# Performance work log

Measured on AMD Instinct MI355X. Metric: run time of the kernel, lower is better.

## Reference

```python
import jax, jax.numpy as jnp
import numpy as np

EPS = 1e-5
K = 16
D = 2

def _bn(x, gamma, beta):
    # eval-mode BatchNorm with running_mean=0, running_var=1
    return x * (gamma / jnp.sqrt(1.0 + EPS)) + beta

def _dense(x, W, b, gamma=None, beta=None, act=True):
    y = x @ W + b
    if act:
        y = jax.nn.elu(y)
    if gamma is not None:
        y = _bn(y, gamma, beta)
    return y

def setup_inputs() -> dict:
    key = jax.random.key(0)
    ks = jax.random.split(key, 16)
    N, Npts, P, dims = 16, 8192, 2048, 3
    C_in, C_out = 64, 128
    C_mid = C_out // 4      # 32
    C_half = C_out // 2     # 64
    dm = 2                  # depth_multiplier = min(ceil(C_out/C_in), 4)
    Ccat = C_mid + C_half   # 96
    def w(k, shape, fan_in):
        return (jax.random.normal(k, shape, jnp.float32) / np.float32(np.sqrt(fan_in)))
    return {
        "rep_pts": jax.random.normal(ks[0], (N, P, dims), jnp.float32),
        "pts": jax.random.normal(ks[1], (N, Npts, dims), jnp.float32),
        "fts": jax.random.normal(ks[2], (N, Npts, C_in), jnp.float32),
        "pts_idx": jax.random.randint(ks[3], (N, P, K * D), 0, Npts),
        # PointCNN.dense: C_in -> C_out//2 (Linear+ELU+BN)
        "dense_W": w(ks[4], (C_in, C_half), C_in), "dense_b": jnp.zeros(C_half),
        "dense_g": jnp.ones(C_half), "dense_bt": jnp.zeros(C_half),
        # XConv dense1/dense2: dims->C_mid->C_mid
        "d1_W": w(ks[5], (dims, C_mid), dims), "d1_b": jnp.zeros(C_mid),
        "d1_g": jnp.ones(C_mid), "d1_bt": jnp.zeros(C_mid),
        "d2_W": w(ks[6], (C_mid, C_mid), C_mid), "d2_b": jnp.zeros(C_mid),
        "d2_g": jnp.ones(C_mid), "d2_bt": jnp.zeros(C_mid),
        "xt_cW": w(ks[7], (K * K, dims, K), dims * K), "xt_cb": jnp.zeros(K * K),
        "xt_d1W": w(ks[8], (K * K, K * K), K * K), "xt_d1b": jnp.zeros(K * K),
        "xt_d2W": w(ks[9], (K * K, K * K), K * K), "xt_d2b": jnp.zeros(K * K),
        # end_conv SepConv: depthwise (1,K) with depth_multiplier, then pointwise 1x1
        "dw_W": w(ks[10], (Ccat, dm, K), K), "dw_b": jnp.zeros(Ccat * dm),
        "pw_W": w(ks[11], (Ccat * dm, C_out), Ccat * dm), "pw_b": jnp.zeros(C_out),
        "sep_g": jnp.ones(C_out), "sep_bt": jnp.zeros(C_out),
    }

def reference(rep_pts, pts, fts, pts_idx,
              dense_W, dense_b, dense_g, dense_bt,
              d1_W, d1_b, d1_g, d1_bt,
              d2_W, d2_b, d2_g, d2_bt,
              xt_cW, xt_cb, xt_d1W, xt_d1b, xt_d2W, xt_d2b,
              dw_W, dw_b, pw_W, pw_b, sep_g, sep_bt):
    idx = pts_idx[:, :, : K * D : D]                  # [N,P,K]
    gather = jax.vmap(lambda a, i: a[i])              # per-batch neighbor gather
    # fts -> Dense(C_in, C_out//2)
    fts_l = _dense(fts, dense_W, dense_b, dense_g, dense_bt)
    pts_reg = gather(pts, idx)                        # [N,P,K,dims]
    fts_reg = gather(fts_l, idx)                      # [N,P,K,C_half]
    pts_local = pts_reg - rep_pts[:, :, None, :]      # center neighborhoods
    # lift coordinates to C_mid features
    l0 = _dense(pts_local, d1_W, d1_b, d1_g, d1_bt)
    lifted = _dense(l0, d2_W, d2_b, d2_g, d2_bt)      # [N,P,K,C_mid]
    fts_cat = jnp.concatenate([lifted, fts_reg], axis=-1)  # [N,P,K,Ccat]
    # X-transform: Conv (1,K) over dims -> K*K (ELU, no BN), two Dense (last no act)
    Xc = jax.nn.elu(jnp.einsum('npkd,odk->npo', pts_local, xt_cW) + xt_cb)
    X = jax.nn.elu(Xc @ xt_d1W + xt_d1b)
    X = X @ xt_d2W + xt_d2b
    N_, P_ = X.shape[0], X.shape[1]
    X = X.reshape(N_, P_, K, K)
    fts_X = jnp.einsum('npij,npjc->npic', X, fts_cat)  # [N,P,K,Ccat]
    # depthwise separable conv over K, then ELU + BN, squeeze -> [N,P,C_out]
    dw = jnp.einsum('npkc,cmk->npcm', fts_X, dw_W).reshape(N_, P_, -1) + dw_b
    out = jax.nn.elu(dw @ pw_W + pw_b)
    out = _bn(out, sep_g, sep_bt)
    return out
```

## Files before the change

### kernel.cpp

```cpp
#include <hip/hip_runtime.h>
#include <hip/hip_bf16.h>

#define RS 0.9999950000374998f

__device__ __forceinline__ float eluf(float x) {
    return x > 0.0f ? x : __expf(x) - 1.0f;
}

typedef __attribute__((ext_vector_type(8))) __bf16 bf16x8;
typedef __attribute__((ext_vector_type(4))) float f32x4;
typedef __attribute__((ext_vector_type(4))) unsigned int u32x4;

__global__ __launch_bounds__(256) void gather_kernel(
    const float* __restrict__ rep_pts, const float* __restrict__ pts,
    const int* __restrict__ pts_idx, const float* __restrict__ d1W,
    const float* __restrict__ d2W, const float* __restrict__ pwW,
    const float* __restrict__ d2Ws, const float* __restrict__ denseW,
    const float* __restrict__ cW, float* __restrict__ pts_local,
    __hip_bfloat16* __restrict__ PLB, __hip_bfloat16* __restrict__ d1Wt,
    __hip_bfloat16* __restrict__ d2Wt, __hip_bfloat16* __restrict__ pwWt,
    __hip_bfloat16* __restrict__ d2pWt, __hip_bfloat16* __restrict__ denseWt,
    __hip_bfloat16* __restrict__ cWt) {
    const int tid = threadIdx.x;
    if (blockIdx.x < 256) {
        const int t = blockIdx.x * 256 + tid;
        {
            const int k = t >> 8, n = t & 255;
            d1Wt[n * 256 + k] = __float2bfloat16(d1W[t]);
            d2Wt[n * 256 + k] = __float2bfloat16(d2W[t]);
        }
        if (t < 24576) {
            const int k = t >> 7, n = t & 127;
            pwWt[n * 192 + k] = __float2bfloat16(pwW[t]);
        }
        if (t < 1024) {
            const int q = t >> 5, c = t & 31;
            d2pWt[c * 32 + q] = __float2bfloat16(d2Ws[t]);
        }
        if (t < 4096) {
            const int k = t >> 6, n = t & 63;
            denseWt[n * 64 + k] = __float2bfloat16(denseW[t]);
        }
        if (t < 16384) {
            const int o = t >> 6, kq = t & 63;
            cWt[t] = (kq < 48) ? __float2bfloat16(cW[o * 48 + kq])
                               : __float2bfloat16(0.0f);
        }
    }
    const long gp0 = (long)blockIdx.x * 16;
    const int pt = tid >> 4, k = tid & 15;
    const long gp = gp0 + pt;
    const int n = (int)(gp >> 11);
    const int idx = pts_idx[gp * 32 + 2 * k];
    const float* ps = pts + ((long)n * 8192 + idx) * 3;
    const float* rs = rep_pts + gp * 3;
#pragma unroll
    for (int d = 0; d < 3; ++d) {
        const float v = ps[d] - rs[d];
        pts_local[gp * 48 + k * 3 + d] = v;
        PLB[gp * 64 + d * 16 + k] = __float2bfloat16(v);
    }
    PLB[gp * 64 + 48 + k] = __float2bfloat16(0.0f);
}

__global__ __launch_bounds__(256) void mfma_gemm_f32a64(
    const float* __restrict__ A, const __hip_bfloat16* __restrict__ Wt,
    const float* __restrict__ bias, const float* __restrict__ gamma,
    const float* __restrict__ beta, __hip_bfloat16* __restrict__ outp, int K,
    int Ncols) {
    __shared__ __bf16 As[128][40];
    __shared__ __bf16 Bs[64][40];
    const int tid = threadIdx.x;
    const int w = tid >> 6, l = tid & 63;
    const long row0 = (long)blockIdx.x * 128;
    const int sr = tid >> 1, sh = tid & 1;
    const int fr = l & 15, kg = (l >> 4) * 8;
    f32x4 acc[2][4] = {};
    const float* __restrict__ ap = A + (row0 + sr) * (long)K + sh * 16;
    const __hip_bfloat16* __restrict__ bp = Wt + (long)(sr & 63) * K + sh * 16;
    for (int k0 = 0; k0 < K; k0 += 32) {
        float av[16];
#pragma unroll
        for (int q = 0; q < 4; ++q) {
            const float4 v = *reinterpret_cast<const float4*>(ap + k0 + q * 4);
            av[q * 4 + 0] = v.x;
            av[q * 4 + 1] = v.y;
            av[q * 4 + 2] = v.z;
            av[q * 4 + 3] = v.w;
        }
        union {
            __bf16 b[16];
            uint4 u[2];
        } cv;
#pragma unroll
        for (int e = 0; e < 16; ++e) cv.b[e] = (__bf16)av[e];
        *reinterpret_cast<uint4*>(&As[sr][sh * 16]) = cv.u[0];
        *reinterpret_cast<uint4*>(&As[sr][sh * 16 + 8]) = cv.u[1];
        if (tid < 128) {
            const uint4 bv0 = *reinterpret_cast<const uint4*>(bp + k0);
            const uint4 bv1 = *reinterpret_cast<const uint4*>(bp + k0 + 8);
            *reinterpret_cast<uint4*>(&Bs[sr & 63][sh * 16]) = bv0;
            *reinterpret_cast<uint4*>(&Bs[sr & 63][sh * 16 + 8]) = bv1;
        }
        __syncthreads();
        bf16x8 af[2], bfv[4];
#pragma unroll
        for (int mt = 0; mt < 2; ++mt)
            af[mt] =
                *reinterpret_cast<const bf16x8*>(&As[w * 32 + mt * 16 + fr][kg]);
#pragma unroll
        for (int nt = 0; nt < 4; ++nt)
            bfv[nt] = *reinterpret_cast<const bf16x8*>(&Bs[nt * 16 + fr][kg]);
#pragma unroll
        for (int mt = 0; mt < 2; ++mt)
#pragma unroll
            for (int nt = 0; nt < 4; ++nt)
                acc[mt][nt] = __builtin_amdgcn_mfma_f32_16x16x32_bf16(
                    af[mt], bfv[nt], acc[mt][nt], 0, 0, 0);
        __syncthreads();
    }
    const int rg = (l >> 4) * 4;
#pragma unroll
    for (int nt = 0; nt < 4; ++nt) {
        const int col = nt * 16 + fr;
        const float bb = bias[col];
        const float gs = gamma[col] * RS;
        const float bt = beta[col];
#pragma unroll
        for (int mt = 0; mt < 2; ++mt) {
#pragma unroll
            for (int r = 0; r < 4; ++r) {
                const long row = row0 + w * 32 + mt * 16 + rg + r;
                float v = acc[mt][nt][r] + bb;
                v = eluf(v) * gs + bt;
                outp[row * Ncols + col] = __float2bfloat16(v);
            }
        }
    }
}

__global__ __launch_bounds__(1024) void xchain_kernel(
    const __hip_bfloat16* __restrict__ PLB, const __hip_bfloat16* __restrict__ cWt,
    const float* __restrict__ cb, const __hip_bfloat16* __restrict__ d1Wt,
    const float* __restrict__ d1b, const __hip_bfloat16* __restrict__ d2Wt,
    const float* __restrict__ d2b, __hip_bfloat16* __restrict__ X2B) {
    __shared__ __bf16 Ap[128][264];
    __shared__ __bf16 Bs[256][40];
    const int tid = threadIdx.x;
    const int w = tid >> 6, l = tid & 63;
    const int wm = w >> 2, wn = w & 3;
    const long row0 = (long)blockIdx.x * 128;
    const int fr = l & 15, kg = (l >> 4) * 8, rg = (l >> 4) * 4;

    {
        const int r = tid >> 3, q = tid & 7;
        *reinterpret_cast<uint4*>(&Ap[r][q * 8]) =
            *reinterpret_cast<const uint4*>(PLB + (row0 + r) * 64 + q * 8);
    }
    __syncthreads();

    auto layer = [&](const __hip_bfloat16* __restrict__ Wt,
                     const float* __restrict__ bias, int K, bool act,
                     bool last) {
        f32x4 acc[2][4] = {};
        for (int k0 = 0; k0 < K; k0 += 32) {
            {
                const int col = tid >> 2, q = tid & 3;
                *reinterpret_cast<uint4*>(&Bs[col][q * 8]) =
                    *reinterpret_cast<const uint4*>(Wt + (long)col * K + k0 +
                                                    q * 8);
            }
            __syncthreads();
            bf16x8 af[2], bfv[4];
#pragma unroll
            for (int mt = 0; mt < 2; ++mt)
                af[mt] = *reinterpret_cast<const bf16x8*>(
                    &Ap[wm * 32 + mt * 16 + fr][k0 + kg]);
#pragma unroll
            for (int nt = 0; nt < 4; ++nt)
                bfv[nt] = *reinterpret_cast<const bf16x8*>(
                    &Bs[wn * 64 + nt * 16 + fr][kg]);
#pragma unroll
            for (int mt = 0; mt < 2; ++mt)
#pragma unroll
                for (int nt = 0; nt < 4; ++nt)
                    acc[mt][nt] = __builtin_amdgcn_mfma_f32_16x16x32_bf16(
                        af[mt], bfv[nt], acc[mt][nt], 0, 0, 0);
            __syncthreads();
        }
#pragma unroll
        for (int nt = 0; nt < 4; ++nt) {
            const int col = wn * 64 + nt * 16 + fr;
            const float bb = bias[col];
#pragma unroll
            for (int mt = 0; mt < 2; ++mt) {
#pragma unroll
                for (int r = 0; r < 4; ++r) {
                    const int row = wm * 32 + mt * 16 + rg + r;
                    float v = acc[mt][nt][r] + bb;
                    if (act) v = eluf(v);
                    const __bf16 h = (__bf16)v;
                    if (last)
                        X2B[(row0 + row) * 256 + col] =
                            *reinterpret_cast<const __hip_bfloat16*>(&h);
                    else
                        Ap[row][col] = h;
                }
            }
        }
        __syncthreads();
    };

    layer(cWt, cb, 64, true, false);
    layer(d1Wt, d1b, 256, true, false);
    layer(d2Wt, d2b, 256, false, true);
}

__global__ __launch_bounds__(1024) void final_stage_kernel(
    const __hip_bfloat16* __restrict__ X2B,
    const float* __restrict__ pts_local,
    const int* __restrict__ pts_idx,
    const __hip_bfloat16* __restrict__ fts_lB,
    const float* __restrict__ d1_W, const float* __restrict__ d1_b,
    const float* __restrict__ d1_g, const float* __restrict__ d1_bt,
    const __hip_bfloat16* __restrict__ d2pWt,
    const float* __restrict__ d2_b, const float* __restrict__ d2_g,
    const float* __restrict__ d2_bt, const float* __restrict__ dw_W,
    const float* __restrict__ dw_b,
    const __hip_bfloat16* __restrict__ pwWt,
    const float* __restrict__ pw_b, const float* __restrict__ sep_g,
    const float* __restrict__ sep_bt,
    float* __restrict__ out)
{
    __shared__ __bf16 fcatF[16 * 96 * 16];
    __shared__ __bf16 dws[16][200];
    __shared__ float dwT[96][36];
    __shared__ float wd1[6][32];
    __shared__ float d2e[3][32];
    __shared__ float dwbs[192];

    const int tid = threadIdx.x;
    const int w = tid >> 6, l = tid & 63;

    for (int i = tid; i < 3072; i += 1024) dwT[i >> 5][i & 31] = dw_W[i];
    if (tid < 96) wd1[tid >> 5][tid & 31] = d1_W[tid];
    else if (tid < 128) wd1[3][tid & 31] = d1_b[tid & 31];
    else if (tid < 160) wd1[4][tid & 31] = d1_g[tid & 31] * RS;
    else if (tid < 192) wd1[5][tid & 31] = d1_bt[tid & 31];
    else if (tid < 224) d2e[0][tid & 31] = d2_b[tid & 31];
    else if (tid < 256) d2e[1][tid & 31] = d2_g[tid & 31] * RS;
    else if (tid < 288) d2e[2][tid & 31] = d2_bt[tid & 31];
    else if (tid < 480) dwbs[tid - 288] = dw_b[tid - 288];
    __syncthreads();

    const int obid = blockIdx.x;
    const int bid = (obid & 7) * 256 + (obid >> 3);
    const int gp = bid * 16 + w;
    const int ugp = __builtin_amdgcn_readfirstlane(gp);
    const int n = ugp >> 11;
    const int fr = l & 15;
    const int kg = (l >> 4) * 8;
    const int kk = kg & 15;
    const unsigned msk = (l < 32) ? 0xFFFFFFFFu : 0u;
    const int rg4 = (l >> 4) * 4;
    const int colg = (l < 32) ? (32 + l) : (l - 32);
    const __hip_bfloat16* __restrict__ fbase =
        fts_lB + (long)n * 8192 * 64 + colg;

#define FIDX(W, ROW, E) ((((W)*96 + (ROW)) << 4) + ((E) ^ (((ROW)&4) << 1)))

    const int* __restrict__ ip = pts_idx + (long)ugp * 32;
    unsigned fg[16];
#pragma unroll
    for (int j = 0; j < 16; ++j)
        fg[j] = *reinterpret_cast<const unsigned short*>(
            &fbase[(long)ip[2 * j] * 64]);

    const float* __restrict__ pp = pts_local + (long)ugp * 48 + fr * 3;
    const float plA0 = pp[0], plA1 = pp[1], plA2 = pp[2];

    bf16x8 a_l0;
#pragma unroll
    for (int jj = 0; jj < 8; ++jj) {
        const int q = kg + jj;
        float a = wd1[3][q];
        a = fmaf(plA0, wd1[0][q], a);
        a = fmaf(plA1, wd1[1][q], a);
        a = fmaf(plA2, wd1[2][q], a);
        a = eluf(a);
        a = a * wd1[4][q] + wd1[5][q];
        a_l0[jj] = (__bf16)a;
    }

    {
        const bf16x8 b0 =
            *reinterpret_cast<const bf16x8*>(d2pWt + (0 + fr) * 32 + kg);
        const bf16x8 b1 =
            *reinterpret_cast<const bf16x8*>(d2pWt + (16 + fr) * 32 + kg);
        f32x4 lif0 = {}, lif1 = {};
        lif0 = __builtin_amdgcn_mfma_f32_16x16x32_bf16(a_l0, b0, lif0, 0, 0, 0);
        lif1 = __builtin_amdgcn_mfma_f32_16x16x32_bf16(a_l0, b1, lif1, 0, 0, 0);
#pragma unroll
        for (int f = 0; f < 2; ++f) {
            const int c = f * 16 + fr;
            const float bb = d2e[0][c & 31], gs = d2e[1][c & 31],
                        bt = d2e[2][c & 31];
            const f32x4 dd = f ? lif1 : lif0;
            unsigned short pk[4];
#pragma unroll
            for (int r = 0; r < 4; ++r) {
                float v = dd[r] + bb;
                v = eluf(v) * gs + bt;
                const __bf16 h = (__bf16)v;
                pk[r] = *reinterpret_cast<const unsigned short*>(&h);
            }
            *reinterpret_cast<uint2*>(&fcatF[FIDX(w, c, rg4)]) =
                make_uint2((unsigned)pk[0] | ((unsigned)pk[1] << 16),
                           (unsigned)pk[2] | ((unsigned)pk[3] << 16));
        }
    }

    {
        const uint4 lo = make_uint4(fg[0] | (fg[1] << 16), fg[2] | (fg[3] << 16),
                                    fg[4] | (fg[5] << 16), fg[6] | (fg[7] << 16));
        const uint4 hi =
            make_uint4(fg[8] | (fg[9] << 16), fg[10] | (fg[11] << 16),
                       fg[12] | (fg[13] << 16), fg[14] | (fg[15] << 16));
        const int row = 32 + colg;
        *reinterpret_cast<uint4*>(&fcatF[FIDX(w, row, 0)]) = lo;
        *reinterpret_cast<uint4*>(&fcatF[FIDX(w, row, 8)]) = hi;
    }

    u32x4 axu =
        *reinterpret_cast<const u32x4*>(X2B + (long)ugp * 256 + fr * 16 + kk);
    axu &= msk;
    const bf16x8 ax = *reinterpret_cast<const bf16x8*>(&axu);

    f32x4 acc[6];
#pragma unroll
    for (int f = 0; f < 6; ++f) acc[f] = (f32x4){};
#pragma unroll
    for (int f = 0; f < 6; ++f) {
        u32x4 bu =
            *reinterpret_cast<const u32x4*>(&fcatF[FIDX(w, f * 16 + fr, kk)]);
        bu &= msk;
        const bf16x8 bf = *reinterpret_cast<const bf16x8*>(&bu);
        acc[f] = __builtin_amdgcn_mfma_f32_16x16x32_bf16(ax, bf, acc[f], 0, 0, 0);
    }

    float dwv[6][2];
#pragma unroll
    for (int f = 0; f < 6; ++f) {
        const int c = f * 16 + fr;
        const float4 w0 = *reinterpret_cast<const float4*>(&dwT[c][rg4]);
        const float4 w1 = *reinterpret_cast<const float4*>(&dwT[c][16 + rg4]);
        float p0 = acc[f][0] * w0.x;
        p0 = fmaf(acc[f][1], w0.y, p0);
        p0 = fmaf(acc[f][2], w0.z, p0);
        p0 = fmaf(acc[f][3], w0.w, p0);
        float p1 = acc[f][0] * w1.x;
        p1 = fmaf(acc[f][1], w1.y, p1);
        p1 = fmaf(acc[f][2], w1.z, p1);
        p1 = fmaf(acc[f][3], w1.w, p1);
        p0 += __shfl_xor(p0, 16);
        p0 += __shfl_xor(p0, 32);
        p1 += __shfl_xor(p1, 16);
        p1 += __shfl_xor(p1, 32);
        dwv[f][0] = p0;
        dwv[f][1] = p1;
    }
    if (l < 16) {
#pragma unroll
        for (int f = 0; f < 6; ++f) {
            const int c = f * 16 + l;
            __hip_bfloat162 pk;
            pk.x = __float2bfloat16(dwv[f][0] + dwbs[2 * c + 0]);
            pk.y = __float2bfloat16(dwv[f][1] + dwbs[2 * c + 1]);
            *reinterpret_cast<__hip_bfloat162*>(&dws[w][2 * c]) = pk;
        }
    }
    __syncthreads();

    const int c8 = w & 7, h2 = w >> 3;
    f32x4 pacc = {};
#pragma unroll
    for (int t = 0; t < 3; ++t) {
        const int kc = h2 * 3 + t;
        const bf16x8 a =
            *reinterpret_cast<const bf16x8*>(&dws[fr][kc * 32 + kg]);
        const bf16x8 b = *reinterpret_cast<const bf16x8*>(
            pwWt + (long)(c8 * 16 + fr) * 192 + kc * 32 + kg);
        pacc = __builtin_amdgcn_mfma_f32_16x16x32_bf16(a, b, pacc, 0, 0, 0);
    }
    float* red = reinterpret_cast<float*>(fcatF);
    if (w >= 8)
        *reinterpret_cast<f32x4*>(&red[(c8 * 64 + l) * 4]) = pacc;
    __syncthreads();
    if (w < 8) {
        const f32x4 other =
            *reinterpret_cast<const f32x4*>(&red[(c8 * 64 + l) * 4]);
        const int col = c8 * 16 + fr;
        const float bb = pw_b[col];
        const float gs = sep_g[col] * RS;
        const float bt = sep_bt[col];
#pragma unroll
        for (int r = 0; r < 4; ++r) {
            float v = pacc[r] + other[r] + bb;
            v = eluf(v) * gs + bt;
            out[(long)(bid * 16 + rg4 + r) * 128 + col] = v;
        }
    }
#undef FIDX
}

extern "C" void kernel_launch(void* const* d_in, const int* in_sizes, int n_in,
                              void* d_out, int out_size, void* d_ws,
                              size_t ws_size, hipStream_t stream) {
    const float* rep_pts = (const float*)d_in[0];
    const float* pts = (const float*)d_in[1];
    const float* fts = (const float*)d_in[2];
    const int* pts_idx = (const int*)d_in[3];
    const float* dense_W = (const float*)d_in[4];
    const float* dense_b = (const float*)d_in[5];
    const float* dense_g = (const float*)d_in[6];
    const float* dense_bt = (const float*)d_in[7];
    const float* d1_W = (const float*)d_in[8];
    const float* d1_b = (const float*)d_in[9];
    const float* d1_g = (const float*)d_in[10];
    const float* d1_bt = (const float*)d_in[11];
    const float* d2_W = (const float*)d_in[12];
    const float* d2_b = (const float*)d_in[13];
    const float* d2_g = (const float*)d_in[14];
    const float* d2_bt = (const float*)d_in[15];
    const float* xt_cW = (const float*)d_in[16];
    const float* xt_cb = (const float*)d_in[17];
    const float* xt_d1W = (const float*)d_in[18];
    const float* xt_d1b = (const float*)d_in[19];
    const float* xt_d2W = (const float*)d_in[20];
    const float* xt_d2b = (const float*)d_in[21];
    const float* dw_W = (const float*)d_in[22];
    const float* dw_b = (const float*)d_in[23];
    const float* pw_W = (const float*)d_in[24];
    const float* pw_b = (const float*)d_in[25];
    const float* sep_g = (const float*)d_in[26];
    const float* sep_bt = (const float*)d_in[27];

    float* ws = (float*)d_ws;
    __hip_bfloat16* fts_lB = (__hip_bfloat16*)ws;
    __hip_bfloat16* X2Bb = (__hip_bfloat16*)(ws + 8388608);
    __hip_bfloat16* PLB = (__hip_bfloat16*)(ws + 20971520);
    float* pl = ws + 25165824;
    __hip_bfloat16* d1Wt = (__hip_bfloat16*)(ws + 26738688);
    __hip_bfloat16* d2Wt = (__hip_bfloat16*)(ws + 26771456);
    __hip_bfloat16* pwWt = (__hip_bfloat16*)(ws + 26804224);
    __hip_bfloat16* d2pWt = (__hip_bfloat16*)(ws + 26816512);
    __hip_bfloat16* denseWt = (__hip_bfloat16*)(ws + 26817024);
    __hip_bfloat16* cWt = (__hip_bfloat16*)(ws + 26819072);

    gather_kernel<<<2048, 256, 0, stream>>>(
        rep_pts, pts, pts_idx, xt_d1W, xt_d2W, pw_W, d2_W, dense_W, xt_cW, pl,
        PLB, d1Wt, d2Wt, pwWt, d2pWt, denseWt, cWt);

    mfma_gemm_f32a64<<<dim3(1024, 1), 256, 0, stream>>>(
        fts, denseWt, dense_b, dense_g, dense_bt, fts_lB, 64, 64);

    xchain_kernel<<<256, 1024, 0, stream>>>(PLB, cWt, xt_cb, d1Wt, xt_d1b,
                                            d2Wt, xt_d2b, X2Bb);

    final_stage_kernel<<<2048, 1024, 0, stream>>>(
        X2Bb, pl, pts_idx, fts_lB, d1_W, d1_b, d1_g, d1_bt, d2pWt, d2_b, d2_g,
        d2_bt, dw_W, dw_b, pwWt, pw_b, sep_g, sep_bt, (float*)d_out);
}
```

Measured before the change: 90.09 us.

## Fuse point gather with dense feature GEMM and halve xchain block size

Merges the gather/weight-prep kernel and the fts dense GEMM into one launch, split by block index. The GEMM blocks now read and transpose the fp32 dense weights directly, so they no longer wait on a prepared bf16 copy and both jobs can run concurrently. The X-transform chain kernel moves from 1024-thread blocks over 128 rows to 512-thread blocks over 64 rows, with two passes for each weight-tile load. The aim is to cut one launch and its serialization gap and to improve occupancy, at the cost of redundant weight conversion in every GEMM block and more weight traffic per row in xchain.

```diff
diff --git a/kernel.cpp b/kernel.cpp
--- a/kernel.cpp
+++ b/kernel.cpp
@@ -11,74 +11,66 @@
 typedef __attribute__((ext_vector_type(4))) float f32x4;
 typedef __attribute__((ext_vector_type(4))) unsigned int u32x4;
 
-__global__ __launch_bounds__(256) void gather_kernel(
+__global__ __launch_bounds__(256) void prep_kernel(
     const float* __restrict__ rep_pts, const float* __restrict__ pts,
-    const int* __restrict__ pts_idx, const float* __restrict__ d1W,
-    const float* __restrict__ d2W, const float* __restrict__ pwW,
-    const float* __restrict__ d2Ws, const float* __restrict__ denseW,
-    const float* __restrict__ cW, float* __restrict__ pts_local,
+    const int* __restrict__ pts_idx, const float* __restrict__ fts,
+    const float* __restrict__ d1W, const float* __restrict__ d2W,
+    const float* __restrict__ pwW, const float* __restrict__ d2Ws,
+    const float* __restrict__ cW, const float* __restrict__ denseW,
+    const float* __restrict__ dense_b, const float* __restrict__ dense_g,
+    const float* __restrict__ dense_bt, float* __restrict__ pts_local,
     __hip_bfloat16* __restrict__ PLB, __hip_bfloat16* __restrict__ d1Wt,
     __hip_bfloat16* __restrict__ d2Wt, __hip_bfloat16* __restrict__ pwWt,
-    __hip_bfloat16* __restrict__ d2pWt, __hip_bfloat16* __restrict__ denseWt,
-    __hip_bfloat16* __restrict__ cWt) {
+    __hip_bfloat16* __restrict__ d2pWt, __hip_bfloat16* __restrict__ cWt,
+    __hip_bfloat16* __restrict__ fts_lB) {
     const int tid = threadIdx.x;
-    if (blockIdx.x < 256) {
-        const int t = blockIdx.x * 256 + tid;
-        {
-            const int k = t >> 8, n = t & 255;
-            d1Wt[n * 256 + k] = __float2bfloat16(d1W[t]);
-            d2Wt[n * 256 + k] = __float2bfloat16(d2W[t]);
-        }
-        if (t < 24576) {
-            const int k = t >> 7, n = t & 127;
-            pwWt[n * 192 + k] = __float2bfloat16(pwW[t]);
-        }
-        if (t < 1024) {
-            const int q = t >> 5, c = t & 31;
-            d2pWt[c * 32 + q] = __float2bfloat16(d2Ws[t]);
-        }
-        if (t < 4096) {
-            const int k = t >> 6, n = t & 63;
-            denseWt[n * 64 + k] = __float2bfloat16(denseW[t]);
-        }
-        if (t < 16384) {
-            const int o = t >> 6, kq = t & 63;
-            cWt[t] = (kq < 48) ? __float2bfloat16(cW[o * 48 + kq])
-                               : __float2bfloat16(0.0f);
-        }
-    }
-    const long gp0 = (long)blockIdx.x * 16;
-    const int pt = tid >> 4, k = tid & 15;
-    const long gp = gp0 + pt;
-    const int n = (int)(gp >> 11);
-    const int idx = pts_idx[gp * 32 + 2 * k];
-    const float* ps = pts + ((long)n * 8192 + idx) * 3;
-    const float* rs = rep_pts + gp * 3;
-#pragma unroll
-    for (int d = 0; d < 3; ++d) {
-        const float v = ps[d] - rs[d];
-        pts_local[gp * 48 + k * 3 + d] = v;
-        PLB[gp * 64 + d * 16 + k] = __float2bfloat16(v);
-    }
-    PLB[gp * 64 + 48 + k] = __float2bfloat16(0.0f);
-}
-
-__global__ __launch_bounds__(256) void mfma_gemm_f32a64(
-    const float* __restrict__ A, const __hip_bfloat16* __restrict__ Wt,
-    const float* __restrict__ bias, const float* __restrict__ gamma,
-    const float* __restrict__ beta, __hip_bfloat16* __restrict__ outp, int K,
-    int Ncols) {
+    if (blockIdx.x < 2048) {
+        if (blockIdx.x < 256) {
+            const int t = blockIdx.x * 256 + tid;
+            {
+                const int k = t >> 8, n = t & 255;
+                d1Wt[n * 256 + k] = __float2bfloat16(d1W[t]);
+                d2Wt[n * 256 + k] = __float2bfloat16(d2W[t]);
+            }
+            if (t < 24576) {
+                const int k = t >> 7, n = t & 127;
+                pwWt[n * 192 + k] = __float2bfloat16(pwW[t]);
+            }
+            if (t < 1024) {
+                const int q = t >> 5, c = t & 31;
+                d2pWt[c * 32 + q] = __float2bfloat16(d2Ws[t]);
+            }
+            if (t < 16384) {
+                const int o = t >> 6, kq = t & 63;
+                cWt[t] = (kq < 48) ? __float2bfloat16(cW[o * 48 + kq])
+                                   : __float2bfloat16(0.0f);
+            }
+        }
+        const long gp0 = (long)blockIdx.x * 16;
+        const int pt = tid >> 4, k = tid & 15;
+        const long gp = gp0 + pt;
+        const int n = (int)(gp >> 11);
+        const int idx = pts_idx[gp * 32 + 2 * k];
+        const float* ps = pts + ((long)n * 8192 + idx) * 3;
+        const float* rs = rep_pts + gp * 3;
+#pragma unroll
+        for (int d = 0; d < 3; ++d) {
+            const float v = ps[d] - rs[d];
+            pts_local[gp * 48 + k * 3 + d] = v;
+            PLB[gp * 64 + d * 16 + k] = __float2bfloat16(v);
+        }
+        PLB[gp * 64 + 48 + k] = __float2bfloat16(0.0f);
+        return;
+    }
     __shared__ __bf16 As[128][40];
     __shared__ __bf16 Bs[64][40];
-    const int tid = threadIdx.x;
     const int w = tid >> 6, l = tid & 63;
-    const long row0 = (long)blockIdx.x * 128;
+    const long row0 = (long)(blockIdx.x - 2048) * 128;
     const int sr = tid >> 1, sh = tid & 1;
     const int fr = l & 15, kg = (l >> 4) * 8;
     f32x4 acc[2][4] = {};
-    const float* __restrict__ ap = A + (row0 + sr) * (long)K + sh * 16;
-    const __hip_bfloat16* __restrict__ bp = Wt + (long)(sr & 63) * K + sh * 16;
-    for (int k0 = 0; k0 < K; k0 += 32) {
+    const float* __restrict__ ap = fts + (row0 + sr) * 64 + sh * 16;
+    for (int k0 = 0; k0 < 64; k0 += 32) {
         float av[16];
 #pragma unroll
         for (int q = 0; q < 4; ++q) {
@@ -96,11 +88,11 @@
         for (int e = 0; e < 16; ++e) cv.b[e] = (__bf16)av[e];
         *reinterpret_cast<uint4*>(&As[sr][sh * 16]) = cv.u[0];
         *reinterpret_cast<uint4*>(&As[sr][sh * 16 + 8]) = cv.u[1];
-        if (tid < 128) {
-            const uint4 bv0 = *reinterpret_cast<const uint4*>(bp + k0);
-            const uint4 bv1 = *reinterpret_cast<const uint4*>(bp + k0 + 8);
-            *reinterpret_cast<uint4*>(&Bs[sr & 63][sh * 16]) = bv0;
-            *reinterpret_cast<uint4*>(&Bs[sr & 63][sh * 16 + 8]) = bv1;
+#pragma unroll
+        for (int s = 0; s < 8; ++s) {
+            const int e = s * 256 + tid;
+            const int kx = e >> 6, col = e & 63;
+            Bs[col][kx] = (__bf16)denseW[(k0 + kx) * 64 + col];
         }
         __syncthreads();
         bf16x8 af[2], bfv[4];
@@ -123,9 +115,9 @@
 #pragma unroll
     for (int nt = 0; nt < 4; ++nt) {
         const int col = nt * 16 + fr;
-        const float bb = bias[col];
-        const float gs = gamma[col] * RS;
-        const float bt = beta[col];
+        const float bb = dense_b[col];
+        const float gs = dense_g[col] * RS;
+        const float bt = dense_bt[col];
 #pragma unroll
         for (int mt = 0; mt < 2; ++mt) {
 #pragma unroll
@@ -133,23 +125,23 @@
                 const long row = row0 + w * 32 + mt * 16 + rg + r;
                 float v = acc[mt][nt][r] + bb;
                 v = eluf(v) * gs + bt;
-                outp[row * Ncols + col] = __float2bfloat16(v);
+                fts_lB[row * 64 + col] = __float2bfloat16(v);
             }
         }
     }
 }
 
-__global__ __launch_bounds__(1024) void xchain_kernel(
+__global__ __launch_bounds__(512) void xchain_kernel(
     const __hip_bfloat16* __restrict__ PLB, const __hip_bfloat16* __restrict__ cWt,
     const float* __restrict__ cb, const __hip_bfloat16* __restrict__ d1Wt,
     const float* __restrict__ d1b, const __hip_bfloat16* __restrict__ d2Wt,
     const float* __restrict__ d2b, __hip_bfloat16* __restrict__ X2B) {
-    __shared__ __bf16 Ap[128][264];
+    __shared__ __bf16 Ap[64][264];
     __shared__ __bf16 Bs[256][40];
     const int tid = threadIdx.x;
     const int w = tid >> 6, l = tid & 63;
     const int wm = w >> 2, wn = w & 3;
-    const long row0 = (long)blockIdx.x * 128;
+    const long row0 = (long)blockIdx.x * 64;
     const int fr = l & 15, kg = (l >> 4) * 8, rg = (l >> 4) * 4;
 
     {
@@ -164,8 +156,10 @@
                      bool last) {
         f32x4 acc[2][4] = {};
         for (int k0 = 0; k0 < K; k0 += 32) {
-            {
-                const int col = tid >> 2, q = tid & 3;
+#pragma unroll
+            for (int s = 0; s < 2; ++s) {
+                const int i = s * 512 + tid;
+                const int col = i >> 2, q = i & 3;
                 *reinterpret_cast<uint4*>(&Bs[col][q * 8]) =
                     *reinterpret_cast<const uint4*>(Wt + (long)col * K + k0 +
                                                     q * 8);
@@ -454,18 +448,15 @@
     __hip_bfloat16* d2Wt = (__hip_bfloat16*)(ws + 26771456);
     __hip_bfloat16* pwWt = (__hip_bfloat16*)(ws + 26804224);
     __hip_bfloat16* d2pWt = (__hip_bfloat16*)(ws + 26816512);
-    __hip_bfloat16* denseWt = (__hip_bfloat16*)(ws + 26817024);
     __hip_bfloat16* cWt = (__hip_bfloat16*)(ws + 26819072);
 
-    gather_kernel<<<2048, 256, 0, stream>>>(
-        rep_pts, pts, pts_idx, xt_d1W, xt_d2W, pw_W, d2_W, dense_W, xt_cW, pl,
-        PLB, d1Wt, d2Wt, pwWt, d2pWt, denseWt, cWt);
-
-    mfma_gemm_f32a64<<<dim3(1024, 1), 256, 0, stream>>>(
-        fts, denseWt, dense_b, dense_g, dense_bt, fts_lB, 64, 64);
-
-    xchain_kernel<<<256, 1024, 0, stream>>>(PLB, cWt, xt_cb, d1Wt, xt_d1b,
-                                            d2Wt, xt_d2b, X2Bb);
+    prep_kernel<<<3072, 256, 0, stream>>>(
+        rep_pts, pts, pts_idx, fts, xt_d1W, xt_d2W, pw_W, d2_W, xt_cW, dense_W,
+        dense_b, dense_g, dense_bt, pl, PLB, d1Wt, d2Wt, pwWt, d2pWt, cWt,
+        fts_lB);
+
+    xchain_kernel<<<512, 512, 0, stream>>>(PLB, cWt, xt_cb, d1Wt, xt_d1b, d2Wt,
+                                           xt_d2b, X2Bb);
 
     final_stage_kernel<<<2048, 1024, 0, stream>>>(
         X2Bb, pl, pts_idx, fts_lB, d1_W, d1_b, d1_g, d1_bt, d2pWt, d2_b, d2_g,
```

Measured after the change: 87.27 us, median of 4. -3.1%, faster.
